# Performance work log

Hardware: AMD Instinct MI355X
Metric: run time of the kernel (lower is better)

The kernel has to match this reference:

```python
import jax, jax.numpy as jnp
import numpy as np

SCALES = (0.9, 1.1)


def resize_bilinear(x, oh, ow):
    """Bilinear resize matching torch F.interpolate(mode='bilinear', align_corners=False).
    x: [B, C, H, W] -> [B, C, oh, ow]."""
    B, C, H, W = x.shape
    if (oh, ow) == (H, W):
        return x
    ys = jnp.clip((jnp.arange(oh, dtype=jnp.float32) + 0.5) * (H / oh) - 0.5, 0.0, H - 1)
    xs = jnp.clip((jnp.arange(ow, dtype=jnp.float32) + 0.5) * (W / ow) - 0.5, 0.0, W - 1)
    y0 = jnp.floor(ys).astype(jnp.int32)
    x0 = jnp.floor(xs).astype(jnp.int32)
    y1 = jnp.minimum(y0 + 1, H - 1)
    x1 = jnp.minimum(x0 + 1, W - 1)
    wy = (ys - y0).astype(x.dtype)[None, None, :, None]
    wx = (xs - x0).astype(x.dtype)[None, None, None, :]
    row = x[:, :, y0, :] * (1 - wy) + x[:, :, y1, :] * wy   # [B,C,oh,W]
    out = row[:, :, :, x0] * (1 - wx) + row[:, :, :, x1] * wx  # [B,C,oh,ow]
    return out


def xcorr_same(feat, filt):
    """F.conv2d cross-correlation with asymmetric 'same' padding as in compute_similarity_scores.
    feat: [1, C, H, W], filt: [N, C, FH, FW] -> [1, N, H, W]."""
    FH, FW = filt.shape[2], filt.shape[3]
    pad = ((FH // 2, (FH - 1) // 2), (FW // 2, (FW - 1) // 2))
    return jax.lax.conv_general_dilated(
        feat, filt, window_strides=(1, 1), padding=pad,
        dimension_numbers=('NCHW', 'OIHW', 'NCHW'))


def scale_boxes(tlbr_np, sh, sw, HF, WF):
    """rescale_box_features: floor top/left, ceil bottom/right, +1 and clamp to feature bounds."""
    t = np.maximum(np.floor(tlbr_np[:, 0] * sh), 0)
    l = np.maximum(np.floor(tlbr_np[:, 1] * sw), 0)
    b = np.minimum(np.ceil(tlbr_np[:, 2] * sh) + 1, HF)
    r = np.minimum(np.ceil(tlbr_np[:, 3] * sw) + 1, WF)
    return np.stack([t, l, b, r], axis=1).astype(np.int32)


def scaled_size(h, w, s):
    hs = int(np.ceil(h * s)); hs = h if hs <= 1 else hs
    ws = int(np.ceil(w * s)); ws = w if ws <= 1 else ws
    return hs, ws


def image_similarities(m3, m4, tlbr_np, img_h, img_w):
    """m3: [512,H3,W3], m4: [1024,H4,W4], tlbr_np: [N,4] int. Returns [6, N, H3, W3]."""
    sims = []
    for feat in (m3, m4):
        C, HF, WF = feat.shape
        sb = scale_boxes(tlbr_np, HF / img_h, WF / img_w, HF, WF)
        crops = [feat[:, t:b, l:r] for t, l, b, r in sb]  # variable-size ROI crops
        mh = max(c.shape[1] for c in crops)
        mw = max(c.shape[2] for c in crops)
        patches = jnp.concatenate(
            [resize_bilinear(c[None], mh, mw) for c in crops], axis=0)  # [N,C,mh,mw]
        sizes = [(mh, mw)] + [scaled_size(mh, mw, s) for s in SCALES]
        for (hs, ws) in sizes:
            filt = resize_bilinear(patches, hs, ws)
            sims.append(xcorr_same(feat[None], filt))  # [1,N,HF,WF]
    # resize_to_uniform_height_width over the 6 similarity maps, then cat on dim0
    mh = max(s.shape[2] for s in sims)
    mw = max(s.shape[3] for s in sims)
    return jnp.concatenate([resize_bilinear(s, mh, mw) for s in sims], axis=0)  # [6,N,mh,mw]


def setup_inputs() -> dict:
    key = jax.random.key(0)
    k3, k4 = jax.random.split(key)
    B, N = 4, 3
    map3 = jax.random.normal(k3, (B, 512, 128, 128), dtype=jnp.float32)
    map4 = jax.random.normal(k4, (B, 1024, 64, 64), dtype=jnp.float32)
    base = np.array([[100, 120, 220, 260],
                     [400,  80, 520, 230],
                     [600, 640, 740, 790]], dtype=np.int32)
    tlbr = jnp.asarray(np.stack([base + 8 * i for i in range(B)], axis=0))  # [B,N,4]
    return {"map3": map3, "map4": map4, "tlbr": tlbr, "img_h": 1024, "img_w": 1024}


def reference(map3, map4, tlbr, img_h, img_w):
    tlbr_np = np.asarray(tlbr)  # box coords are host-side constants (shapes depend on them)
    B = map3.shape[0]
    outs = [image_similarities(map3[i], map4[i], tlbr_np[i], img_h, img_w) for i in range(B)]
    out = jnp.stack(outs, axis=0)          # [B, 6, N, H, W]
    return jnp.transpose(out, (0, 2, 1, 3, 4))  # [B, N, 6, H, W]
```

## Files before the change

kernel.cpp:

```cpp
#include <hip/hip_runtime.h>
#include <math.h>

typedef float  fx4  __attribute__((ext_vector_type(4)));
typedef short  bfx8 __attribute__((ext_vector_type(8)));

__device__ __forceinline__ void bl_w(int o, int O, int I, int& i0, int& i1, float& w) {
    float r = (float)((double)I / (double)O);
    float f = (o + 0.5f) * r - 0.5f;
    f = fminf(fmaxf(f, 0.0f), (float)(I - 1));
    int a = (int)floorf(f);
    i0 = a;
    i1 = min(a + 1, I - 1);
    w = f - (float)a;
}

__device__ __forceinline__ unsigned int bf16rne(float f) {
    unsigned int x = __builtin_bit_cast(unsigned int, f);
    return ((x + 0x7fffu + ((x >> 16) & 1u)) >> 16) & 0xffffu;
}

__device__ __forceinline__ unsigned int pk_bf16(float lo, float hi) {
    unsigned int r;
    asm("v_cvt_pk_bf16_f32 %0, %1, %2" : "=v"(r) : "v"(lo), "v"(hi));
    return r;
}

__global__ void k_meta(const int* __restrict__ tlbr, const int* __restrict__ p_imgh,
                       const int* __restrict__ p_imgw, int B, int N, int ms,
                       int* __restrict__ meta) {
    if (blockIdx.x != 0 || threadIdx.x != 0) return;
    const int HFs[2] = {128, 64};
    const double SC[2] = {0.9, 1.1};
    int img_h = *p_imgh, img_w = *p_imgw;
    for (int b = 0; b < B; ++b)
      for (int lvl = 0; lvl < 2; ++lvl) {
        int HF = HFs[lvl], WF = HFs[lvl];
        double sh = (double)HF / (double)img_h;
        double sw = (double)WF / (double)img_w;
        int* m = meta + (b*2 + lvl)*ms;
        int mh = 0, mw = 0;
        for (int n = 0; n < N; ++n) {
            const int* bx = tlbr + ((size_t)(b*N) + n)*4;
            int t  = max((int)floor((double)bx[0]*sh), 0);
            int l  = max((int)floor((double)bx[1]*sw), 0);
            int bb = min((int)ceil((double)bx[2]*sh) + 1, HF);
            int rr = min((int)ceil((double)bx[3]*sw) + 1, WF);
            int chh = bb - t, cww = rr - l;
            m[2+4*n+0] = t; m[2+4*n+1] = l; m[2+4*n+2] = chh; m[2+4*n+3] = cww;
            mh = max(mh, chh); mw = max(mw, cww);
        }
        m[0] = mh; m[1] = mw;
        int fo = 2 + 4*N;
        m[fo+0] = mh; m[fo+1] = mw;
        for (int s = 0; s < 2; ++s) {
            int hs  = (int)ceil((double)mh * SC[s]); if (hs  <= 1) hs  = mh;
            int wsv = (int)ceil((double)mw * SC[s]); if (wsv <= 1) wsv = mw;
            m[fo+2+2*s] = hs; m[fo+2+2*s+1] = wsv;
        }
      }
}

template<int C, int KH, int KW, int NKYG>
__global__ void k_filters(const float* __restrict__ feat_all, const int* __restrict__ meta,
                          unsigned short* __restrict__ Wswz, int b0, int chunkB,
                          int N, int lvl, int ms, int HF, int WF) {
    constexpr int KWG = KW/4;
    constexpr int KT  = C*KWG*NKYG;
    long long idx = (long long)blockIdx.x*256 + threadIdx.x;
    long long total = (long long)chunkB * KT * 256;
    if (idx >= total) return;
    int jj = ((int)(idx & 3)) * 2;
    int m  = (int)((idx >> 2) & 15);
    int g  = (int)((idx >> 6) & 3);
    long long rest = idx >> 8;
    int s  = (int)(rest % KT);
    int lb = (int)(rest / KT);
    int kyg = s % NKYG; int s2 = s / NKYG;
    int kxg = s2 % KWG;
    int c   = s2 / KWG;
    int kx  = kxg*4 + g;
    int ky  = kyg*8 + jj;
    unsigned int outv = 0;
    int sc = m / N, n = m - sc*N;
    if (sc < 3) {
        int b = b0 + lb;
        const int* mt = meta + (b*2 + lvl)*ms;
        int mh = mt[0], mw = mt[1];
        int t = mt[2+4*n], l = mt[3+4*n], chh = mt[4+4*n], cww = mt[5+4*n];
        int fo = 2 + 4*N;
        int fh = mt[fo + 2*sc], fw = mt[fo + 2*sc + 1];
        int offy = KH/2 - fh/2, offx = KW/2 - fw/2;
        int fx = kx - offx;
        if (fx >= 0 && fx < fw) {
            const float* src = feat_all + ((size_t)b*C + c)*HF*WF;
            int px0, px1; float wx;
            bl_w(fx, fw, mw, px0, px1, wx);
            int ax0, ax1; float awx; bl_w(px0, mw, cww, ax0, ax1, awx);
            int bx0, bx1; float bwx; bl_w(px1, mw, cww, bx0, bx1, bwx);
            #pragma unroll
            for (int q = 0; q < 2; ++q) {
                int fy = ky + q - offy;
                if (fy >= 0 && fy < fh) {
                    int py0, py1; float wy;
                    bl_w(fy, fh, mh, py0, py1, wy);
                    float pv[2][2];
                    #pragma unroll
                    for (int pi = 0; pi < 2; ++pi) {
                        int py = pi ? py1 : py0;
                        int cy0, cy1; float cwy;
                        bl_w(py, mh, chh, cy0, cy1, cwy);
                        const float* r0 = src + (size_t)(t + cy0)*WF + l;
                        const float* r1 = src + (size_t)(t + cy1)*WF + l;
                        pv[pi][0] = (r0[ax0]*(1.f-cwy) + r1[ax0]*cwy)*(1.f-awx)
                                  + (r0[ax1]*(1.f-cwy) + r1[ax1]*cwy)*awx;
                        pv[pi][1] = (r0[bx0]*(1.f-cwy) + r1[bx0]*cwy)*(1.f-bwx)
                                  + (r0[bx1]*(1.f-cwy) + r1[bx1]*cwy)*bwx;
                    }
                    float v = (pv[0][0]*(1.f-wy) + pv[1][0]*wy)*(1.f-wx)
                            + (pv[0][1]*(1.f-wy) + pv[1][1]*wy)*wx;
                    outv |= bf16rne(v) << (16*q);
                }
            }
        }
    }
    ((unsigned int*)Wswz)[idx] = outv;
}

template<int C, int KS, int KH, int KW, int H, int W, int NKYG, int NDY,
         int CC, int RSTR, int NCOL, int P>
__global__ __launch_bounds__(256, 5) void k_mfconv(
        const float* __restrict__ feat_all, const unsigned short* __restrict__ Wswz,
        float* __restrict__ part, int b0, int Btot, int N, int nks) {
    constexpr int KWG   = KW/4;
    constexpr int CHSTR = NCOL*RSTR;
    constexpr int NROWS = KH + (NDY-1)*8;
    constexpr int NRT   = NROWS/8;
    constexpr int NCT   = NCOL/4;
    constexpr int KT    = C*KWG*NKYG;
    constexpr int NFR   = NKYG + NDY - 1;
    __shared__ __align__(16) unsigned short smem[CC*CHSTR];

    const int xb  = blockIdx.x;
    const int yb  = blockIdx.y;
    const int zz  = blockIdx.z;
    const int ksp = zz % nks;
    const int lb  = zz / nks;
    const int b   = b0 + lb;
    const int y0  = (yb >> 3)*(8*NDY) + (yb & 7);
    const int tid = threadIdx.x;
    const int lane = tid & 63;
    const int wv   = tid >> 6;
    const int g    = lane >> 4;
    const int lm   = lane & 15;

    fx4 acc[NDY];
    #pragma unroll
    for (int t = 0; t < NDY; ++t) acc[t] = (fx4){0.f, 0.f, 0.f, 0.f};

    const float* feat = feat_all + (size_t)b * C * H * W;
    const unsigned short* Wlane = Wswz + ((size_t)lb*KT)*512 + lane*8;
    const int bcol0 = (wv*16 + lm + g)*RSTR;

    for (int cb_ = 0; cb_ < KS; cb_ += CC) {
        const int c0 = ksp*KS + cb_;
        for (int it = tid; it < CC*NCT*NRT; it += 256) {
            int rt = it % NRT; int t2 = it / NRT;
            int ct = t2 % NCT; int ch = t2 / NCT;
            const float* src = feat + (size_t)(c0 + ch)*H*W;
            int col0 = ct*4, r0 = rt*8;
            int x0 = xb*64 + col0 - P;
            float4 f[8];
            #pragma unroll
            for (int rr = 0; rr < 8; ++rr) {
                int y = y0 + r0 + rr - P;
                bool yok = (y >= 0) && (y < H);
                if (yok && x0 >= 0 && x0 + 3 < W) {
                    f[rr] = *reinterpret_cast<const float4*>(src + (size_t)y*W + x0);
                } else {
                    float t4[4];
                    #pragma unroll
                    for (int j = 0; j < 4; ++j) {
                        int x = x0 + j;
                        t4[j] = (yok && x >= 0 && x < W) ? src[(size_t)y*W + x] : 0.f;
                    }
                    f[rr] = make_float4(t4[0], t4[1], t4[2], t4[3]);
                }
            }
            #pragma unroll
            for (int j = 0; j < 4; ++j) {
                uint4 w4;
                w4.x = pk_bf16(((const float*)&f[0])[j], ((const float*)&f[1])[j]);
                w4.y = pk_bf16(((const float*)&f[2])[j], ((const float*)&f[3])[j]);
                w4.z = pk_bf16(((const float*)&f[4])[j], ((const float*)&f[5])[j]);
                w4.w = pk_bf16(((const float*)&f[6])[j], ((const float*)&f[7])[j]);
                *reinterpret_cast<uint4*>(smem + ch*CHSTR + (col0 + j)*RSTR + r0) = w4;
            }
        }
        __syncthreads();
        #pragma unroll 1
        for (int ch = 0; ch < CC; ++ch) {
            const unsigned short* Wc = Wlane + ((size_t)(c0 + ch)*KWG*NKYG)*512;
            const unsigned short* sb = smem + ch*CHSTR;
            #pragma unroll 2
            for (int kxg = 0; kxg < KWG; ++kxg) {
                bfx8 af[NKYG];
                #pragma unroll
                for (int kyg = 0; kyg < NKYG; ++kyg)
                    af[kyg] = *reinterpret_cast<const bfx8*>(Wc + (size_t)(kxg*NKYG + kyg)*512);
                const unsigned short* bp = sb + bcol0 + kxg*4*RSTR;
                bfx8 fr[NFR];
                #pragma unroll
                for (int rg = 0; rg < NFR; ++rg)
                    fr[rg] = *reinterpret_cast<const bfx8*>(bp + rg*8);
                __builtin_amdgcn_s_setprio(1);
                #pragma unroll
                for (int dy = 0; dy < NDY; ++dy)
                    #pragma unroll
                    for (int kyg = 0; kyg < NKYG; ++kyg)
                        acc[dy] = __builtin_amdgcn_mfma_f32_16x16x32_bf16(
                            af[kyg], fr[kyg + dy], acc[dy], 0, 0, 0);
                __builtin_amdgcn_s_setprio(0);
            }
        }
        __syncthreads();
    }
    const int x = xb*64 + wv*16 + lm;
    #pragma unroll
    for (int dy = 0; dy < NDY; ++dy) {
        int y = y0 + dy*8;
        if (y >= H) continue;
        #pragma unroll
        for (int r = 0; r < 4; ++r) {
            int m  = g*4 + r;
            int sc = m / N;
            int n  = m - sc*N;
            if (sc < 3) {
                size_t oi = ((((size_t)ksp*Btot + b)*N + n)*3 + sc)*((size_t)H*W)
                          + (size_t)y*W + x;
                part[oi] = acc[dy][r];
            }
        }
    }
}

__global__ void k_reduce3(const float* __restrict__ part, float* __restrict__ out,
                          int B, int N, int nks) {
    int idx = blockIdx.x*256 + threadIdx.x;
    int tot = B*N*3*128*128;
    if (idx >= tot) return;
    int px = idx & 16383;
    int r = idx >> 14;
    int sc = r % 3; r /= 3;
    int n = r % N; int b = r / N;
    size_t stride = (size_t)B*N*3*16384;
    const float* p = part + ((size_t)(b*N + n)*3 + sc)*16384 + px;
    float s = 0.f;
    for (int ks = 0; ks < nks; ++ks) s += p[(size_t)ks*stride];
    out[(((size_t)(b*N + n)*6 + sc) << 14) + px] = s;
}

__global__ void k_upsample_sum(const float* __restrict__ part, float* __restrict__ out,
                               int B, int N, int nks) {
    int idx = blockIdx.x*256 + threadIdx.x;
    int tot = B*N*3*128*128;
    if (idx >= tot) return;
    int x = idx & 127; int r = idx >> 7;
    int y = r & 127; r >>= 7;
    int sc = r % 3; r /= 3;
    int n = r % N; int b = r / N;
    int y0, y1, x0, x1; float wy, wx;
    bl_w(y, 128, 64, y0, y1, wy);
    bl_w(x, 128, 64, x0, x1, wx);
    size_t stride = (size_t)B*N*3*4096;
    const float* p = part + ((size_t)(b*N + n)*3 + sc)*4096;
    float f00 = 0.f, f10 = 0.f, f01 = 0.f, f11 = 0.f;
    for (int ks = 0; ks < nks; ++ks) {
        const float* q = p + (size_t)ks*stride;
        f00 += q[y0*64 + x0]; f10 += q[y1*64 + x0];
        f01 += q[y0*64 + x1]; f11 += q[y1*64 + x1];
    }
    out[((size_t)((b*N + n)*6 + 3 + sc)*128 + y)*128 + x] =
        (f00*(1.f-wy) + f10*wy)*(1.f-wx) + (f01*(1.f-wy) + f11*wy)*wx;
}

extern "C" void kernel_launch(void* const* d_in, const int* in_sizes, int n_in,
                              void* d_out, int out_size, void* d_ws, size_t ws_size,
                              hipStream_t stream) {
    const float* map3 = (const float*)d_in[0];
    const float* map4 = (const float*)d_in[1];
    const int*   tlbr = (const int*)d_in[2];
    const int*   p_imgh = (const int*)d_in[3];
    const int*   p_imgw = (const int*)d_in[4];
    float* out = (float*)d_out;

    const int C3 = 512, H3 = 128, C4 = 1024, H4 = 64;
    int B = in_sizes[0] / (C3 * H3 * H3);
    int N = in_sizes[2] / (B * 4);
    int ms = 2 + 4 * N + 6;
    const int NKS3 = 16, NKS4 = 64;

    char* wsp = (char*)d_ws;
    int* meta = (int*)wsp;
    size_t off = 4096;
    float* part = (float*)(wsp + off);
    size_t part_bytes = (size_t)NKS3 * B * N * 3 * H3 * H3 * 4;
    off += part_bytes;
    unsigned short* Wbuf = (unsigned short*)(wsp + off);
    size_t wavail = (ws_size > off) ? (ws_size - off) : 0;
    size_t wpb = (size_t)9216 * 1024;
    int cb = (int)(wavail / wpb); if (cb > B) cb = B; if (cb < 1) cb = 1;

    k_meta<<<1, 1, 0, stream>>>(tlbr, p_imgh, p_imgw, B, N, ms, meta);

    {
        for (int b0 = 0; b0 < B; b0 += cb) {
            int cbn = (cb < B - b0) ? cb : (B - b0);
            long long pr = (long long)cbn * 9216 * 256;
            k_filters<512,24,24,3><<<(int)((pr + 255) / 256), 256, 0, stream>>>(
                map3, meta, Wbuf, b0, cbn, N, 0, ms, H3, H3);
            dim3 grid(2, 16, cbn * NKS3);
            k_mfconv<512,32,24,24,128,128,3,8,2,88,88,12><<<grid, 256, 0, stream>>>(
                map3, Wbuf, part, b0, B, N, NKS3);
        }
        int tot = B * N * 3 * H3 * H3;
        k_reduce3<<<(tot + 255) / 256, 256, 0, stream>>>(part, out, B, N, NKS3);
    }
    {
        for (int b0 = 0; b0 < B; b0 += cb) {
            int cbn = (cb < B - b0) ? cb : (B - b0);
            long long pr = (long long)cbn * 8192 * 256;
            k_filters<1024,16,16,2><<<(int)((pr + 255) / 256), 256, 0, stream>>>(
                map4, meta, Wbuf, b0, cbn, N, 1, ms, H4, H4);
            dim3 grid(1, 8, cbn * NKS4);
            k_mfconv<1024,16,16,16,64,64,2,8,2,72,80,8><<<grid, 256, 0, stream>>>(
                map4, Wbuf, part, b0, B, N, NKS4);
        }
        int tot = B * N * 3 * H3 * H3;
        k_upsample_sum<<<(tot + 255) / 256, 256, 0, stream>>>(part, out, B, N, NKS4);
    }
}
```

Before: 991.1 us.

## Restructure MFMA conv: full-width tiles, per-channel staging, prefetched weights, precomputed resize ratios

The filter-building kernel now precomputes resize ratios in the metadata kernel and has each thread produce eight bf16 taps written as one 16-byte store, which cuts double-precision divisions and thread count. The MFMA convolution now covers the full image width per block (NT column tiles) with fewer row groups. It stages one channel at a time into LDS, prefetches the next channel's weight fragments into registers while computing, and rotates the channel start order per block to spread memory traffic. The trade-offs are more accumulator registers (launch bounds lowered to 4 blocks), two barriers per channel, and a different grid shape.

```diff
diff --git a/kernel.cpp b/kernel.cpp
--- a/kernel.cpp
+++ b/kernel.cpp
@@ -6,6 +6,15 @@
 
 __device__ __forceinline__ void bl_w(int o, int O, int I, int& i0, int& i1, float& w) {
     float r = (float)((double)I / (double)O);
+    float f = (o + 0.5f) * r - 0.5f;
+    f = fminf(fmaxf(f, 0.0f), (float)(I - 1));
+    int a = (int)floorf(f);
+    i0 = a;
+    i1 = min(a + 1, I - 1);
+    w = f - (float)a;
+}
+
+__device__ __forceinline__ void bl_w_r(int o, float r, int I, int& i0, int& i1, float& w) {
     float f = (o + 0.5f) * r - 0.5f;
     f = fminf(fmaxf(f, 0.0f), (float)(I - 1));
     int a = (int)floorf(f);
@@ -57,6 +66,16 @@
             int wsv = (int)ceil((double)mw * SC[s]); if (wsv <= 1) wsv = mw;
             m[fo+2+2*s] = hs; m[fo+2+2*s+1] = wsv;
         }
+        int fo2 = fo + 6;
+        for (int s = 0; s < 3; ++s) {
+            int fh = m[fo+2*s], fw = m[fo+2*s+1];
+            m[fo2+2*s]   = __float_as_int((float)((double)mw / (double)fw));
+            m[fo2+2*s+1] = __float_as_int((float)((double)mh / (double)fh));
+        }
+        for (int n = 0; n < N; ++n) {
+            m[fo2+6+2*n]   = __float_as_int((float)((double)m[2+4*n+3] / (double)mw));
+            m[fo2+6+2*n+1] = __float_as_int((float)((double)m[2+4*n+2] / (double)mh));
+        }
       }
 }
 
@@ -66,21 +85,21 @@
                           int N, int lvl, int ms, int HF, int WF) {
     constexpr int KWG = KW/4;
     constexpr int KT  = C*KWG*NKYG;
-    long long idx = (long long)blockIdx.x*256 + threadIdx.x;
-    long long total = (long long)chunkB * KT * 256;
-    if (idx >= total) return;
-    int jj = ((int)(idx & 3)) * 2;
-    int m  = (int)((idx >> 2) & 15);
-    int g  = (int)((idx >> 6) & 3);
-    long long rest = idx >> 8;
+    long long tau = (long long)blockIdx.x*256 + threadIdx.x;
+    long long total = (long long)chunkB * KT * 64;
+    if (tau >= total) return;
+    int m  = (int)(tau & 15);
+    int g  = (int)((tau >> 4) & 3);
+    long long rest = tau >> 6;
     int s  = (int)(rest % KT);
     int lb = (int)(rest / KT);
     int kyg = s % NKYG; int s2 = s / NKYG;
     int kxg = s2 % KWG;
     int c   = s2 / KWG;
     int kx  = kxg*4 + g;
-    int ky  = kyg*8 + jj;
-    unsigned int outv = 0;
+    int ky0 = kyg*8;
+    uint4 outv = make_uint4(0, 0, 0, 0);
+    unsigned int* ow = (unsigned int*)&outv;
     int sc = m / N, n = m - sc*N;
     if (sc < 3) {
         int b = b0 + lb;
@@ -89,58 +108,58 @@
         int t = mt[2+4*n], l = mt[3+4*n], chh = mt[4+4*n], cww = mt[5+4*n];
         int fo = 2 + 4*N;
         int fh = mt[fo + 2*sc], fw = mt[fo + 2*sc + 1];
+        int fo2 = fo + 6;
+        float r1 = __int_as_float(mt[fo2+2*sc]);
+        float r2 = __int_as_float(mt[fo2+2*sc+1]);
+        float r3 = __int_as_float(mt[fo2+6+2*n]);
+        float r4 = __int_as_float(mt[fo2+6+2*n+1]);
         int offy = KH/2 - fh/2, offx = KW/2 - fw/2;
         int fx = kx - offx;
         if (fx >= 0 && fx < fw) {
             const float* src = feat_all + ((size_t)b*C + c)*HF*WF;
-            int px0, px1; float wx;
-            bl_w(fx, fw, mw, px0, px1, wx);
-            int ax0, ax1; float awx; bl_w(px0, mw, cww, ax0, ax1, awx);
-            int bx0, bx1; float bwx; bl_w(px1, mw, cww, bx0, bx1, bwx);
+            int px0, px1; float wx;  bl_w_r(fx, r1, mw, px0, px1, wx);
+            int ax0, ax1; float awx; bl_w_r(px0, r3, cww, ax0, ax1, awx);
+            int bx0, bx1; float bwx; bl_w_r(px1, r3, cww, bx0, bx1, bwx);
             #pragma unroll
-            for (int q = 0; q < 2; ++q) {
-                int fy = ky + q - offy;
+            for (int jj = 0; jj < 8; ++jj) {
+                int fy = ky0 + jj - offy;
                 if (fy >= 0 && fy < fh) {
-                    int py0, py1; float wy;
-                    bl_w(fy, fh, mh, py0, py1, wy);
+                    int py0, py1; float wy; bl_w_r(fy, r2, mh, py0, py1, wy);
                     float pv[2][2];
                     #pragma unroll
                     for (int pi = 0; pi < 2; ++pi) {
                         int py = pi ? py1 : py0;
-                        int cy0, cy1; float cwy;
-                        bl_w(py, mh, chh, cy0, cy1, cwy);
-                        const float* r0 = src + (size_t)(t + cy0)*WF + l;
-                        const float* r1 = src + (size_t)(t + cy1)*WF + l;
-                        pv[pi][0] = (r0[ax0]*(1.f-cwy) + r1[ax0]*cwy)*(1.f-awx)
-                                  + (r0[ax1]*(1.f-cwy) + r1[ax1]*cwy)*awx;
-                        pv[pi][1] = (r0[bx0]*(1.f-cwy) + r1[bx0]*cwy)*(1.f-bwx)
-                                  + (r0[bx1]*(1.f-cwy) + r1[bx1]*cwy)*bwx;
+                        int cy0, cy1; float cwy; bl_w_r(py, r4, chh, cy0, cy1, cwy);
+                        const float* q0 = src + (size_t)(t + cy0)*WF + l;
+                        const float* q1 = src + (size_t)(t + cy1)*WF + l;
+                        pv[pi][0] = (q0[ax0]*(1.f-cwy) + q1[ax0]*cwy)*(1.f-awx)
+                                  + (q0[ax1]*(1.f-cwy) + q1[ax1]*cwy)*awx;
+                        pv[pi][1] = (q0[bx0]*(1.f-cwy) + q1[bx0]*cwy)*(1.f-bwx)
+                                  + (q0[bx1]*(1.f-cwy) + q1[bx1]*cwy)*bwx;
                     }
                     float v = (pv[0][0]*(1.f-wy) + pv[1][0]*wy)*(1.f-wx)
                             + (pv[0][1]*(1.f-wy) + pv[1][1]*wy)*wx;
-                    outv |= bf16rne(v) << (16*q);
+                    ow[jj >> 1] |= bf16rne(v) << (16*(jj & 1));
                 }
             }
         }
     }
-    ((unsigned int*)Wswz)[idx] = outv;
-}
-
-template<int C, int KS, int KH, int KW, int H, int W, int NKYG, int NDY,
-         int CC, int RSTR, int NCOL, int P>
-__global__ __launch_bounds__(256, 5) void k_mfconv(
+    ((uint4*)Wswz)[tau] = outv;
+}
+
+template<int C, int KS, int KH, int KW, int H, int W, int NKYG, int NDY, int NT,
+         int RSTR, int NCOL, int P>
+__global__ __launch_bounds__(256, 4) void k_mfconv(
         const float* __restrict__ feat_all, const unsigned short* __restrict__ Wswz,
         float* __restrict__ part, int b0, int Btot, int N, int nks) {
     constexpr int KWG   = KW/4;
-    constexpr int CHSTR = NCOL*RSTR;
     constexpr int NROWS = KH + (NDY-1)*8;
     constexpr int NRT   = NROWS/8;
     constexpr int NCT   = NCOL/4;
     constexpr int KT    = C*KWG*NKYG;
     constexpr int NFR   = NKYG + NDY - 1;
-    __shared__ __align__(16) unsigned short smem[CC*CHSTR];
-
-    const int xb  = blockIdx.x;
+    __shared__ __align__(16) unsigned short smem[NCOL*RSTR];
+
     const int yb  = blockIdx.y;
     const int zz  = blockIdx.z;
     const int ksp = zz % nks;
@@ -152,62 +171,82 @@
     const int wv   = tid >> 6;
     const int g    = lane >> 4;
     const int lm   = lane & 15;
-
-    fx4 acc[NDY];
+    const int rot  = (zz*7 + yb*3) & (KS-1);
+
+    fx4 acc[NT][NDY];
     #pragma unroll
-    for (int t = 0; t < NDY; ++t) acc[t] = (fx4){0.f, 0.f, 0.f, 0.f};
+    for (int t = 0; t < NT; ++t)
+        #pragma unroll
+        for (int dy = 0; dy < NDY; ++dy) acc[t][dy] = (fx4){0.f, 0.f, 0.f, 0.f};
 
     const float* feat = feat_all + (size_t)b * C * H * W;
     const unsigned short* Wlane = Wswz + ((size_t)lb*KT)*512 + lane*8;
-    const int bcol0 = (wv*16 + lm + g)*RSTR;
-
-    for (int cb_ = 0; cb_ < KS; cb_ += CC) {
-        const int c0 = ksp*KS + cb_;
-        for (int it = tid; it < CC*NCT*NRT; it += 256) {
-            int rt = it % NRT; int t2 = it / NRT;
-            int ct = t2 % NCT; int ch = t2 / NCT;
-            const float* src = feat + (size_t)(c0 + ch)*H*W;
-            int col0 = ct*4, r0 = rt*8;
-            int x0 = xb*64 + col0 - P;
-            float4 f[8];
-            #pragma unroll
-            for (int rr = 0; rr < 8; ++rr) {
-                int y = y0 + r0 + rr - P;
-                bool yok = (y >= 0) && (y < H);
-                if (yok && x0 >= 0 && x0 + 3 < W) {
-                    f[rr] = *reinterpret_cast<const float4*>(src + (size_t)y*W + x0);
-                } else {
-                    float t4[4];
-                    #pragma unroll
-                    for (int j = 0; j < 4; ++j) {
-                        int x = x0 + j;
-                        t4[j] = (yok && x >= 0 && x < W) ? src[(size_t)y*W + x] : 0.f;
-                    }
-                    f[rr] = make_float4(t4[0], t4[1], t4[2], t4[3]);
+
+    const bool sact = tid < NCT*NRT;
+    const int rt = tid % NRT, ct = tid / NRT;
+    const int col0 = ct*4, r0 = rt*8;
+    const int sx0 = col0 - P;
+
+    auto STAGE = [&](int c) {
+        if (!sact) return;
+        const float* src = feat + (size_t)c*H*W;
+        float4 f[8];
+        #pragma unroll
+        for (int rr = 0; rr < 8; ++rr) {
+            int y = y0 + r0 + rr - P;
+            bool yok = (y >= 0) && (y < H);
+            if (yok && sx0 >= 0 && sx0 + 3 < W) {
+                f[rr] = *reinterpret_cast<const float4*>(src + (size_t)y*W + sx0);
+            } else {
+                float t4[4];
+                #pragma unroll
+                for (int j = 0; j < 4; ++j) {
+                    int x = sx0 + j;
+                    t4[j] = (yok && x >= 0 && x < W) ? src[(size_t)y*W + x] : 0.f;
                 }
-            }
-            #pragma unroll
-            for (int j = 0; j < 4; ++j) {
-                uint4 w4;
-                w4.x = pk_bf16(((const float*)&f[0])[j], ((const float*)&f[1])[j]);
-                w4.y = pk_bf16(((const float*)&f[2])[j], ((const float*)&f[3])[j]);
-                w4.z = pk_bf16(((const float*)&f[4])[j], ((const float*)&f[5])[j]);
-                w4.w = pk_bf16(((const float*)&f[6])[j], ((const float*)&f[7])[j]);
-                *reinterpret_cast<uint4*>(smem + ch*CHSTR + (col0 + j)*RSTR + r0) = w4;
-            }
-        }
-        __syncthreads();
-        #pragma unroll 1
-        for (int ch = 0; ch < CC; ++ch) {
-            const unsigned short* Wc = Wlane + ((size_t)(c0 + ch)*KWG*NKYG)*512;
-            const unsigned short* sb = smem + ch*CHSTR;
-            #pragma unroll 2
-            for (int kxg = 0; kxg < KWG; ++kxg) {
-                bfx8 af[NKYG];
+                f[rr] = make_float4(t4[0], t4[1], t4[2], t4[3]);
+            }
+        }
+        #pragma unroll
+        for (int j = 0; j < 4; ++j) {
+            uint4 w4;
+            w4.x = pk_bf16(((const float*)&f[0])[j], ((const float*)&f[1])[j]);
+            w4.y = pk_bf16(((const float*)&f[2])[j], ((const float*)&f[3])[j]);
+            w4.z = pk_bf16(((const float*)&f[4])[j], ((const float*)&f[5])[j]);
+            w4.w = pk_bf16(((const float*)&f[6])[j], ((const float*)&f[7])[j]);
+            *reinterpret_cast<uint4*>(smem + (col0 + j)*RSTR + r0) = w4;
+        }
+    };
+    auto CHOF = [&](int i) { return ksp*KS + ((i + rot) & (KS-1)); };
+
+    STAGE(CHOF(0));
+    bfx8 afc[NKYG];
+    {
+        const unsigned short* W0 = Wlane + ((size_t)CHOF(0)*KWG)*NKYG*512;
+        #pragma unroll
+        for (int kyg = 0; kyg < NKYG; ++kyg)
+            afc[kyg] = *reinterpret_cast<const bfx8*>(W0 + (size_t)kyg*512);
+    }
+    __syncthreads();
+
+    #pragma unroll 1
+    for (int ci = 0; ci < KS; ++ci) {
+        #pragma unroll 2
+        for (int kxg = 0; kxg < KWG; ++kxg) {
+            bfx8 afn[NKYG];
+            {
+                int ni = (kxg + 1 < KWG) ? ci : ci + 1;
+                int nk = (kxg + 1 < KWG) ? kxg + 1 : 0;
+                const unsigned short* Wn =
+                    Wlane + (((size_t)CHOF(ni)*KWG + nk)*NKYG)*512;
                 #pragma unroll
                 for (int kyg = 0; kyg < NKYG; ++kyg)
-                    af[kyg] = *reinterpret_cast<const bfx8*>(Wc + (size_t)(kxg*NKYG + kyg)*512);
-                const unsigned short* bp = sb + bcol0 + kxg*4*RSTR;
+                    afn[kyg] = *reinterpret_cast<const bfx8*>(Wn + (size_t)kyg*512);
+            }
+            #pragma unroll
+            for (int t = 0; t < NT; ++t) {
+                const unsigned short* bp =
+                    smem + ((size_t)(t*64 + wv*16 + lm + g + kxg*4))*RSTR;
                 bfx8 fr[NFR];
                 #pragma unroll
                 for (int rg = 0; rg < NFR; ++rg)
@@ -217,27 +256,33 @@
                 for (int dy = 0; dy < NDY; ++dy)
                     #pragma unroll
                     for (int kyg = 0; kyg < NKYG; ++kyg)
-                        acc[dy] = __builtin_amdgcn_mfma_f32_16x16x32_bf16(
-                            af[kyg], fr[kyg + dy], acc[dy], 0, 0, 0);
+                        acc[t][dy] = __builtin_amdgcn_mfma_f32_16x16x32_bf16(
+                            afc[kyg], fr[kyg + dy], acc[t][dy], 0, 0, 0);
                 __builtin_amdgcn_s_setprio(0);
             }
+            #pragma unroll
+            for (int kyg = 0; kyg < NKYG; ++kyg) afc[kyg] = afn[kyg];
         }
         __syncthreads();
-    }
-    const int x = xb*64 + wv*16 + lm;
+        if (ci + 1 < KS) STAGE(CHOF(ci + 1));
+        __syncthreads();
+    }
     #pragma unroll
-    for (int dy = 0; dy < NDY; ++dy) {
-        int y = y0 + dy*8;
-        if (y >= H) continue;
-        #pragma unroll
-        for (int r = 0; r < 4; ++r) {
-            int m  = g*4 + r;
-            int sc = m / N;
-            int n  = m - sc*N;
-            if (sc < 3) {
-                size_t oi = ((((size_t)ksp*Btot + b)*N + n)*3 + sc)*((size_t)H*W)
-                          + (size_t)y*W + x;
-                part[oi] = acc[dy][r];
+    for (int t = 0; t < NT; ++t) {
+        const int x = t*64 + wv*16 + lm;
+        #pragma unroll
+        for (int dy = 0; dy < NDY; ++dy) {
+            int y = y0 + dy*8;
+            #pragma unroll
+            for (int r = 0; r < 4; ++r) {
+                int m  = g*4 + r;
+                int sc = m / N;
+                int n  = m - sc*N;
+                if (sc < 3) {
+                    size_t oi = ((((size_t)ksp*Btot + b)*N + n)*3 + sc)*((size_t)H*W)
+                              + (size_t)y*W + x;
+                    part[oi] = acc[t][dy][r];
+                }
             }
         }
     }
@@ -296,7 +341,7 @@
     const int C3 = 512, H3 = 128, C4 = 1024, H4 = 64;
     int B = in_sizes[0] / (C3 * H3 * H3);
     int N = in_sizes[2] / (B * 4);
-    int ms = 2 + 4 * N + 6;
+    int ms = 2 + 4*N + 6 + 6 + 2*N;
     const int NKS3 = 16, NKS4 = 64;
 
     char* wsp = (char*)d_ws;
@@ -315,11 +360,11 @@
     {
         for (int b0 = 0; b0 < B; b0 += cb) {
             int cbn = (cb < B - b0) ? cb : (B - b0);
-            long long pr = (long long)cbn * 9216 * 256;
-            k_filters<512,24,24,3><<<(int)((pr + 255) / 256), 256, 0, stream>>>(
+            long long thr = (long long)cbn * 9216 * 64;
+            k_filters<512,24,24,3><<<(int)((thr + 255) / 256), 256, 0, stream>>>(
                 map3, meta, Wbuf, b0, cbn, N, 0, ms, H3, H3);
-            dim3 grid(2, 16, cbn * NKS3);
-            k_mfconv<512,32,24,24,128,128,3,8,2,88,88,12><<<grid, 256, 0, stream>>>(
+            dim3 grid(1, 32, cbn * NKS3);
+            k_mfconv<512,32,24,24,128,128,3,4,2,56,152,12><<<grid, 256, 0, stream>>>(
                 map3, Wbuf, part, b0, B, N, NKS3);
         }
         int tot = B * N * 3 * H3 * H3;
@@ -328,11 +373,11 @@
     {
         for (int b0 = 0; b0 < B; b0 += cb) {
             int cbn = (cb < B - b0) ? cb : (B - b0);
-            long long pr = (long long)cbn * 8192 * 256;
-            k_filters<1024,16,16,2><<<(int)((pr + 255) / 256), 256, 0, stream>>>(
+            long long thr = (long long)cbn * 8192 * 64;
+            k_filters<1024,16,16,2><<<(int)((thr + 255) / 256), 256, 0, stream>>>(
                 map4, meta, Wbuf, b0, cbn, N, 1, ms, H4, H4);
             dim3 grid(1, 8, cbn * NKS4);
-            k_mfconv<1024,16,16,16,64,64,2,8,2,72,80,8><<<grid, 256, 0, stream>>>(
+            k_mfconv<1024,16,16,16,64,64,2,8,1,72,80,8><<<grid, 256, 0, stream>>>(
                 map4, Wbuf, part, b0, B, N, NKS4);
         }
         int tot = B * N * 3 * H3 * H3;
```

Result: no change. 996.4 us (+0.5%).
